# Kernel tuning notes

Measured on AMD Instinct MI355X. Metric: run time of the kernel, lower is better.

The kernel has to match this reference:

```python
import jax, jax.numpy as jnp
import numpy as np

BS, N_NODES, SEQ_LEN, IN_C, OUT_C = 16, 50000, 9, 32, 32


def setup_inputs() -> dict:
    key = jax.random.key(0)
    k1, k2, k3 = jax.random.split(key, 3)
    x = jax.random.normal(k1, (BS, N_NODES, IN_C), dtype=jnp.float32)
    indices = jax.random.randint(k2, (N_NODES, SEQ_LEN), 0, N_NODES, dtype=jnp.int64)
    # xavier-uniform for the Linear weight [out, in*(seq_len+1)]
    fan_in = IN_C * (SEQ_LEN + 1)
    limit = jnp.sqrt(6.0 / (fan_in + OUT_C)).astype(jnp.float32)
    W = jax.random.uniform(k3, (OUT_C, fan_in), dtype=jnp.float32, minval=-limit, maxval=limit)
    b = jnp.zeros((OUT_C,), dtype=jnp.float32)
    return {"x": x, "indices": indices, "W": W, "b": b}


def reference(x, indices, W, b):
    # x: [bs, n_nodes, in_c]; indices: [n_nodes, seq_len]
    bs = x.shape[0]
    n_nodes, seq_len = indices.shape
    # spiral gather: [bs, n_nodes*seq_len, in_c] -> [bs, n_nodes, seq_len*in_c]
    g = jnp.take(x, indices.reshape(-1), axis=1).reshape(bs, n_nodes, -1)
    # virtual (global) node feature: max over nodes, broadcast to each node
    gmax = jnp.max(x, axis=1, keepdims=True)  # [bs, 1, in_c]
    gmax = jnp.broadcast_to(gmax, (bs, n_nodes, x.shape[-1]))
    feat = jnp.concatenate([g, gmax], axis=-1)  # [bs, n_nodes, (seq_len+1)*in_c]
    return jnp.einsum('bnf,of->bno', feat, W) + b
```

## Files before the change

kernel.cpp:

```cpp
#include <hip/hip_runtime.h>

#define BS 16
#define NN 50000
#define SEQ 9
#define IC 32
#define OC 32
#define FAN 320
#define GROUPS 64
#define MTILES_PER_B (NN / 16)
#define TPX (2 * MTILES_PER_B)
#define PPX MTILES_PER_B
#define KBLK 1792
#define WPX (KBLK / 8 * 4)
#define WLN (SEQ * 2 * 64 * 4)

typedef __attribute__((ext_vector_type(8))) short short8;
typedef __attribute__((ext_vector_type(4))) float f32x4;
typedef __attribute__((ext_vector_type(4))) unsigned uint32x4;

__device__ __forceinline__ float4 fmax4(float4 a, float4 b) {
  return make_float4(fmaxf(a.x, b.x), fmaxf(a.y, b.y), fmaxf(a.z, b.z), fmaxf(a.w, b.w));
}

__device__ __forceinline__ unsigned pk_bf16(float a, float b) {
  unsigned r;
  asm("v_cvt_pk_bf16_f32 %0, %1, %2" : "=v"(r) : "v"(a), "v"(b));
  return r;
}

__device__ __forceinline__ void split8(const float* v, unsigned* hi, unsigned* lo) {
#pragma unroll
  for (int i = 0; i < 4; i++) {
    float a = v[2 * i], b = v[2 * i + 1];
    unsigned h = pk_bf16(a, b);
    float fa = __builtin_bit_cast(float, h << 16);
    float fb = __builtin_bit_cast(float, h & 0xFFFF0000u);
    lo[i] = pk_bf16(a - fa, b - fb);
    hi[i] = h;
  }
}

union FragU { unsigned u[4]; short8 v; };

__global__ __launch_bounds__(256) void kprep(const float* __restrict__ x,
                                             float* __restrict__ partial,
                                             unsigned* __restrict__ xh) {
  int bg = blockIdx.x;
  int b = bg & 15, g = bg >> 4;
  int t = threadIdx.x;
  int q = t & 7, r = t >> 3;
  const float4* xb = (const float4*)(x + (size_t)b * NN * IC);
  unsigned* xhb = xh ? xh + (size_t)b * NN * 16 : nullptr;
  float4 m = make_float4(-INFINITY, -INFINITY, -INFINITY, -INFINITY);
  for (int n = g * 32 + r; n < NN; n += GROUPS * 32) {
    float4 v = xb[n * 8 + q];
    m = fmax4(m, v);
    if (xhb) {
      uint2 p = make_uint2(pk_bf16(v.x, v.y), pk_bf16(v.z, v.w));
      *(uint2*)&xhb[n * 16 + q * 2] = p;
    }
  }
  __shared__ float4 sm[32][8];
  sm[r][q] = m;
  __syncthreads();
  for (int s = 16; s >= 1; s >>= 1) {
    if (r < s) sm[r][q] = fmax4(sm[r][q], sm[r + s][q]);
    __syncthreads();
  }
  if (t < 8) ((float4*)(partial + bg * IC))[t] = sm[0][t];
}

__global__ __launch_bounds__(256) void kfuse(const float* __restrict__ partial,
                                             const float* __restrict__ W,
                                             const float* __restrict__ bias,
                                             float* __restrict__ gcontrib,
                                             unsigned* __restrict__ wfrag) {
  int t = threadIdx.x;
  if (blockIdx.x < BS) {
    int b = blockIdx.x;
    __shared__ float gmax[IC];
    if (t < IC) {
      float m = -INFINITY;
      for (int g = 0; g < GROUPS; g++) m = fmaxf(m, partial[(g * 16 + b) * IC + t]);
      gmax[t] = m;
    }
    __syncthreads();
    if (t < OC) {
      float acc = bias[t];
#pragma unroll
      for (int c = 0; c < IC; c++) acc += gmax[c] * W[t * FAN + SEQ * IC + c];
      gcontrib[b * OC + t] = acc;
    }
  } else {
    int slot = (blockIdx.x - BS) * 256 + t;
    if (slot >= SEQ * 2 * 64) return;
    int s = slot >> 7, rem = slot & 127;
    int n = rem >> 6, l = rem & 63;
    int o = n * 16 + (l & 15);
    int k0 = s * 32 + (l >> 4) * 8;
    const float* p = W + o * FAN + k0;
#pragma unroll
    for (int i = 0; i < 4; i++)
      wfrag[slot * 4 + i] = pk_bf16(p[2 * i], p[2 * i + 1]);
  }
}

__global__ __launch_bounds__(256, 4) void kmfma_bf(const unsigned* __restrict__ xh,
                                                   const int* __restrict__ idx,
                                                   const float* __restrict__ gcontrib,
                                                   const unsigned* __restrict__ wfrag,
                                                   float* __restrict__ out) {
  __shared__ __align__(16) unsigned wl[WLN];
  __shared__ __align__(16) int sidx[4][144];
  int t = threadIdx.x;
  for (int i = t; i < WLN; i += 256) wl[i] = wfrag[i];
  __syncthreads();

  int bid = blockIdx.x;
  int xcd = bid & 7, slot = bid >> 3;
  int wid = t >> 6, l = t & 63;
  int ws = slot * 4 + wid;
  int lane_lo = l & 15, kg = l >> 4;

  int b0 = xcd, b1 = xcd + 8;
  const unsigned* xb0 = xh + (size_t)b0 * NN * 16;
  const unsigned* xb1 = xh + (size_t)b1 * NN * 16;
  f32x4 gc00 = *(const f32x4*)&gcontrib[b0 * OC + kg * 4];
  f32x4 gc01 = *(const f32x4*)&gcontrib[b0 * OC + 16 + kg * 4];
  f32x4 gc10 = *(const f32x4*)&gcontrib[b1 * OC + kg * 4];
  f32x4 gc11 = *(const f32x4*)&gcontrib[b1 * OC + 16 + kg * 4];

  for (int p = ws; p < PPX; p += WPX) {
    int nb = p * 16;

    if (l < 36) *(int4*)&sidx[wid][l * 4] = *(const int4*)(idx + nb * SEQ + l * 4);
    __builtin_amdgcn_sched_barrier(0);

    int j[SEQ];
#pragma unroll
    for (int s = 0; s < SEQ; s++) j[s] = sidx[wid][lane_lo * SEQ + s];

    f32x4 acc00 = {0.f, 0.f, 0.f, 0.f};
    f32x4 acc01 = {0.f, 0.f, 0.f, 0.f};
    f32x4 acc10 = {0.f, 0.f, 0.f, 0.f};
    f32x4 acc11 = {0.f, 0.f, 0.f, 0.f};

#pragma unroll
    for (int s = 0; s < SEQ; s++) {
      size_t off = (size_t)j[s] * 16 + kg * 4;
      uint32x4 r0 = *(const uint32x4*)(xb0 + off);
      uint32x4 r1 = *(const uint32x4*)(xb1 + off);
      short8 a0 = __builtin_bit_cast(short8, r0);
      short8 a1 = __builtin_bit_cast(short8, r1);
      short8 bh0 = *(const short8*)&wl[(s * 2 + 0) * 256 + (l << 2)];
      short8 bh1 = *(const short8*)&wl[(s * 2 + 1) * 256 + (l << 2)];
      acc00 = __builtin_amdgcn_mfma_f32_16x16x32_bf16(bh0, a0, acc00, 0, 0, 0);
      acc01 = __builtin_amdgcn_mfma_f32_16x16x32_bf16(bh1, a0, acc01, 0, 0, 0);
      acc10 = __builtin_amdgcn_mfma_f32_16x16x32_bf16(bh0, a1, acc10, 0, 0, 0);
      acc11 = __builtin_amdgcn_mfma_f32_16x16x32_bf16(bh1, a1, acc11, 0, 0, 0);
    }

    size_t rb0 = ((size_t)b0 * NN + nb + lane_lo) * OC;
    size_t rb1 = ((size_t)b1 * NN + nb + lane_lo) * OC;
    __builtin_nontemporal_store(acc00 + gc00, (f32x4*)&out[rb0 + kg * 4]);
    __builtin_nontemporal_store(acc01 + gc01, (f32x4*)&out[rb0 + 16 + kg * 4]);
    __builtin_nontemporal_store(acc10 + gc10, (f32x4*)&out[rb1 + kg * 4]);
    __builtin_nontemporal_store(acc11 + gc11, (f32x4*)&out[rb1 + 16 + kg * 4]);
  }
}

__global__ __launch_bounds__(256, 8) void kmfma_f32(const float* __restrict__ x,
                                                    const int* __restrict__ idx,
                                                    const float* __restrict__ gcontrib,
                                                    const unsigned* __restrict__ wfrag,
                                                    float* __restrict__ out) {
  __shared__ __align__(16) unsigned wl[WLN];
  int t = threadIdx.x;
  for (int i = t; i < WLN; i += 256) wl[i] = wfrag[i];
  __syncthreads();

  int bid = blockIdx.x;
  int xcd = bid & 7, slot = bid >> 3;
  int wid = t >> 6, l = t & 63;
  int ws = slot * 4 + wid;
  int lane_lo = l & 15, kg = l >> 4;

  for (int tt = ws; tt < TPX; tt += WPX) {
    int bloc = tt >= MTILES_PER_B;
    int loc = tt - bloc * MTILES_PER_B;
    int b = xcd + 8 * bloc;
    int nb = loc * 16;
    const float* xb = x + (size_t)b * NN * IC;

    int j[SEQ];
    const int* ip = idx + (nb + lane_lo) * SEQ;
#pragma unroll
    for (int s = 0; s < SEQ; s++) j[s] = ip[s];

    f32x4 acc0 = {0.f, 0.f, 0.f, 0.f};
    f32x4 acc1 = {0.f, 0.f, 0.f, 0.f};
#pragma unroll
    for (int s = 0; s < SEQ; s++) {
      const float4* row = (const float4*)(xb + (size_t)j[s] * IC + kg * 8);
      float4 q0 = row[0], q1 = row[1];
      float v[8] = {q0.x, q0.y, q0.z, q0.w, q1.x, q1.y, q1.z, q1.w};
      FragU ah, al;
      split8(v, ah.u, al.u);
      short8 bh0 = *(const short8*)&wl[(s * 2 + 0) * 256 + (l << 2)];
      short8 bh1 = *(const short8*)&wl[(s * 2 + 1) * 256 + (l << 2)];
      acc0 = __builtin_amdgcn_mfma_f32_16x16x32_bf16(ah.v, bh0, acc0, 0, 0, 0);
      acc0 = __builtin_amdgcn_mfma_f32_16x16x32_bf16(al.v, bh0, acc0, 0, 0, 0);
      acc1 = __builtin_amdgcn_mfma_f32_16x16x32_bf16(ah.v, bh1, acc1, 0, 0, 0);
      acc1 = __builtin_amdgcn_mfma_f32_16x16x32_bf16(al.v, bh1, acc1, 0, 0, 0);
    }

    float g0 = gcontrib[b * OC + lane_lo];
    float g1 = gcontrib[b * OC + 16 + lane_lo];
#pragma unroll
    for (int jj = 0; jj < 4; jj++) {
      size_t o = ((size_t)b * NN + nb + kg * 4 + jj) * OC;
      __builtin_nontemporal_store(acc0[jj] + g0, &out[o + lane_lo]);
      __builtin_nontemporal_store(acc1[jj] + g1, &out[o + 16 + lane_lo]);
    }
  }
}

extern "C" void kernel_launch(void* const* d_in, const int* in_sizes, int n_in,
                              void* d_out, int out_size, void* d_ws, size_t ws_size,
                              hipStream_t stream) {
  const float* x = (const float*)d_in[0];
  const int* idx = (const int*)d_in[1];
  const float* W = (const float*)d_in[2];
  const float* bias = (const float*)d_in[3];
  float* out = (float*)d_out;

  const size_t xh_bytes = (size_t)BS * NN * 16 * sizeof(unsigned);
  const size_t tail = (size_t)(BS * GROUPS * IC + BS * OC) * 4 + WLN * 4 + 1024;
  bool big = ws_size >= xh_bytes + tail;

  if (big) {
    unsigned* xh = (unsigned*)d_ws;
    float* partial = (float*)((char*)d_ws + xh_bytes);
    float* gcontrib = partial + BS * GROUPS * IC;
    unsigned* wfrag = (unsigned*)(gcontrib + BS * OC);
    kprep<<<BS * GROUPS, 256, 0, stream>>>(x, partial, xh);
    kfuse<<<BS + 5, 256, 0, stream>>>(partial, W, bias, gcontrib, wfrag);
    kmfma_bf<<<KBLK, 256, 0, stream>>>(xh, idx, gcontrib, wfrag, out);
  } else {
    float* partial = (float*)d_ws;
    float* gcontrib = partial + BS * GROUPS * IC;
    unsigned* wfrag = (unsigned*)(gcontrib + BS * OC);
    kprep<<<BS * GROUPS, 256, 0, stream>>>(x, partial, nullptr);
    kfuse<<<BS + 5, 256, 0, stream>>>(partial, W, bias, gcontrib, wfrag);
    kmfma_f32<<<KBLK, 256, 0, stream>>>(x, idx, gcontrib, wfrag, out);
  }
}
```

Before: 112.7 us.

## Store bf16 x node-major across batch so each gathered node is one contiguous row

The prep kernel now writes the bf16 copy of x in a node-major layout where all 16 batches' features for a node sit in one contiguous 1 KB row. The MFMA kernel maps lanes to batch instead of node, so each wave processes one node for all batches and each spiral gather becomes a single coalesced 1 KB load. The shared-memory index staging and per-XCD batch split are removed, and the grid shrinks to 1024 blocks. This replaces many scattered 64-byte gathers with fewer wide ones. The cost is that output stores become strided across batches and each wave handles less work per iteration.

```diff
diff --git a/kernel.cpp b/kernel.cpp
--- a/kernel.cpp
+++ b/kernel.cpp
@@ -9,9 +9,10 @@
 #define GROUPS 64
 #define MTILES_PER_B (NN / 16)
 #define TPX (2 * MTILES_PER_B)
-#define PPX MTILES_PER_B
 #define KBLK 1792
 #define WPX (KBLK / 8 * 4)
+#define KBLK2 1024
+#define NWAVE2 (KBLK2 * 4)
 #define WLN (SEQ * 2 * 64 * 4)
 
 typedef __attribute__((ext_vector_type(8))) short short8;
@@ -44,20 +45,19 @@
 
 __global__ __launch_bounds__(256) void kprep(const float* __restrict__ x,
                                              float* __restrict__ partial,
-                                             unsigned* __restrict__ xh) {
+                                             unsigned* __restrict__ xh2) {
   int bg = blockIdx.x;
   int b = bg & 15, g = bg >> 4;
   int t = threadIdx.x;
   int q = t & 7, r = t >> 3;
   const float4* xb = (const float4*)(x + (size_t)b * NN * IC);
-  unsigned* xhb = xh ? xh + (size_t)b * NN * 16 : nullptr;
   float4 m = make_float4(-INFINITY, -INFINITY, -INFINITY, -INFINITY);
   for (int n = g * 32 + r; n < NN; n += GROUPS * 32) {
     float4 v = xb[n * 8 + q];
     m = fmax4(m, v);
-    if (xhb) {
+    if (xh2) {
       uint2 p = make_uint2(pk_bf16(v.x, v.y), pk_bf16(v.z, v.w));
-      *(uint2*)&xhb[n * 16 + q * 2] = p;
+      *(uint2*)&xh2[(size_t)n * 256 + (q >> 1) * 64 + b * 4 + (q & 1) * 2] = p;
     }
   }
   __shared__ float4 sm[32][8];
@@ -105,67 +105,48 @@
   }
 }
 
-__global__ __launch_bounds__(256, 4) void kmfma_bf(const unsigned* __restrict__ xh,
+__global__ __launch_bounds__(256, 4) void kmfma_nm(const unsigned* __restrict__ xh2,
                                                    const int* __restrict__ idx,
                                                    const float* __restrict__ gcontrib,
                                                    const unsigned* __restrict__ wfrag,
                                                    float* __restrict__ out) {
   __shared__ __align__(16) unsigned wl[WLN];
-  __shared__ __align__(16) int sidx[4][144];
   int t = threadIdx.x;
   for (int i = t; i < WLN; i += 256) wl[i] = wfrag[i];
   __syncthreads();
 
-  int bid = blockIdx.x;
-  int xcd = bid & 7, slot = bid >> 3;
   int wid = t >> 6, l = t & 63;
-  int ws = slot * 4 + wid;
-  int lane_lo = l & 15, kg = l >> 4;
-
-  int b0 = xcd, b1 = xcd + 8;
-  const unsigned* xb0 = xh + (size_t)b0 * NN * 16;
-  const unsigned* xb1 = xh + (size_t)b1 * NN * 16;
-  f32x4 gc00 = *(const f32x4*)&gcontrib[b0 * OC + kg * 4];
-  f32x4 gc01 = *(const f32x4*)&gcontrib[b0 * OC + 16 + kg * 4];
-  f32x4 gc10 = *(const f32x4*)&gcontrib[b1 * OC + kg * 4];
-  f32x4 gc11 = *(const f32x4*)&gcontrib[b1 * OC + 16 + kg * 4];
-
-  for (int p = ws; p < PPX; p += WPX) {
-    int nb = p * 16;
-
-    if (l < 36) *(int4*)&sidx[wid][l * 4] = *(const int4*)(idx + nb * SEQ + l * 4);
-    __builtin_amdgcn_sched_barrier(0);
-
+  int b = l & 15, kg = l >> 4;
+  f32x4 gc0 = *(const f32x4*)&gcontrib[b * OC + kg * 4];
+  f32x4 gc1 = *(const f32x4*)&gcontrib[b * OC + 16 + kg * 4];
+  size_t outb = (size_t)b * NN;
+
+  int w = __builtin_amdgcn_readfirstlane(blockIdx.x * 4 + wid);
+  for (int n = w; n < NN; n += NWAVE2) {
+    const int* ip = idx + n * SEQ;
     int j[SEQ];
 #pragma unroll
-    for (int s = 0; s < SEQ; s++) j[s] = sidx[wid][lane_lo * SEQ + s];
-
-    f32x4 acc00 = {0.f, 0.f, 0.f, 0.f};
-    f32x4 acc01 = {0.f, 0.f, 0.f, 0.f};
-    f32x4 acc10 = {0.f, 0.f, 0.f, 0.f};
-    f32x4 acc11 = {0.f, 0.f, 0.f, 0.f};
-
+    for (int s = 0; s < SEQ; s++) j[s] = ip[s];
+
+    uint32x4 g[SEQ];
+#pragma unroll
+    for (int s = 0; s < SEQ; s++)
+      g[s] = *(const uint32x4*)(xh2 + (size_t)j[s] * 256 + l * 4);
+
+    f32x4 acc0 = {0.f, 0.f, 0.f, 0.f};
+    f32x4 acc1 = {0.f, 0.f, 0.f, 0.f};
 #pragma unroll
     for (int s = 0; s < SEQ; s++) {
-      size_t off = (size_t)j[s] * 16 + kg * 4;
-      uint32x4 r0 = *(const uint32x4*)(xb0 + off);
-      uint32x4 r1 = *(const uint32x4*)(xb1 + off);
-      short8 a0 = __builtin_bit_cast(short8, r0);
-      short8 a1 = __builtin_bit_cast(short8, r1);
-      short8 bh0 = *(const short8*)&wl[(s * 2 + 0) * 256 + (l << 2)];
-      short8 bh1 = *(const short8*)&wl[(s * 2 + 1) * 256 + (l << 2)];
-      acc00 = __builtin_amdgcn_mfma_f32_16x16x32_bf16(bh0, a0, acc00, 0, 0, 0);
-      acc01 = __builtin_amdgcn_mfma_f32_16x16x32_bf16(bh1, a0, acc01, 0, 0, 0);
-      acc10 = __builtin_amdgcn_mfma_f32_16x16x32_bf16(bh0, a1, acc10, 0, 0, 0);
-      acc11 = __builtin_amdgcn_mfma_f32_16x16x32_bf16(bh1, a1, acc11, 0, 0, 0);
-    }
-
-    size_t rb0 = ((size_t)b0 * NN + nb + lane_lo) * OC;
-    size_t rb1 = ((size_t)b1 * NN + nb + lane_lo) * OC;
-    __builtin_nontemporal_store(acc00 + gc00, (f32x4*)&out[rb0 + kg * 4]);
-    __builtin_nontemporal_store(acc01 + gc01, (f32x4*)&out[rb0 + 16 + kg * 4]);
-    __builtin_nontemporal_store(acc10 + gc10, (f32x4*)&out[rb1 + kg * 4]);
-    __builtin_nontemporal_store(acc11 + gc11, (f32x4*)&out[rb1 + 16 + kg * 4]);
+      short8 a = __builtin_bit_cast(short8, g[s]);
+      short8 w0 = *(const short8*)&wl[(s * 2 + 0) * 256 + (l << 2)];
+      short8 w1 = *(const short8*)&wl[(s * 2 + 1) * 256 + (l << 2)];
+      acc0 = __builtin_amdgcn_mfma_f32_16x16x32_bf16(w0, a, acc0, 0, 0, 0);
+      acc1 = __builtin_amdgcn_mfma_f32_16x16x32_bf16(w1, a, acc1, 0, 0, 0);
+    }
+
+    float* op = out + (outb + n) * OC;
+    *(f32x4*)(op + kg * 4) = acc0 + gc0;
+    *(f32x4*)(op + 16 + kg * 4) = acc1 + gc1;
   }
 }
 
@@ -234,18 +215,18 @@
   const float* bias = (const float*)d_in[3];
   float* out = (float*)d_out;
 
-  const size_t xh_bytes = (size_t)BS * NN * 16 * sizeof(unsigned);
+  const size_t xh_bytes = (size_t)NN * 256 * sizeof(unsigned);
   const size_t tail = (size_t)(BS * GROUPS * IC + BS * OC) * 4 + WLN * 4 + 1024;
   bool big = ws_size >= xh_bytes + tail;
 
   if (big) {
-    unsigned* xh = (unsigned*)d_ws;
+    unsigned* xh2 = (unsigned*)d_ws;
     float* partial = (float*)((char*)d_ws + xh_bytes);
     float* gcontrib = partial + BS * GROUPS * IC;
     unsigned* wfrag = (unsigned*)(gcontrib + BS * OC);
-    kprep<<<BS * GROUPS, 256, 0, stream>>>(x, partial, xh);
+    kprep<<<BS * GROUPS, 256, 0, stream>>>(x, partial, xh2);
     kfuse<<<BS + 5, 256, 0, stream>>>(partial, W, bias, gcontrib, wfrag);
-    kmfma_bf<<<KBLK, 256, 0, stream>>>(xh, idx, gcontrib, wfrag, out);
+    kmfma_nm<<<KBLK2, 256, 0, stream>>>(xh2, idx, gcontrib, wfrag, out);
   } else {
     float* partial = (float*)d_ws;
     float* gcontrib = partial + BS * GROUPS * IC;
```

Result: slower. 155.5 us (+38.1%).
